# Kernel tuning notes

Hardware: AMD Instinct MI355X
Metric: run time of the kernel (lower is better)

The kernel has to match this reference:

```python
import jax, jax.numpy as jnp
import numpy as np

THRESHOLD = 8.0
BN_EPS = 1e-5


def setup_inputs() -> dict:
    key = jax.random.key(0)
    k1, k2 = jax.random.split(key)
    B, C, H, W = 2, 128, 64, 64
    x = jax.random.normal(k1, (B, C, H, W), dtype=jnp.float32)
    W_fc = jax.random.normal(k2, (C, C), dtype=jnp.float32) * (1.0 / np.sqrt(C))
    b_fc = jnp.zeros((C,), dtype=jnp.float32)
    gamma = jnp.ones((C,), dtype=jnp.float32)
    beta = jnp.zeros((C,), dtype=jnp.float32)
    return {"x": x, "W_fc": W_fc, "b_fc": b_fc, "gamma": gamma, "beta": beta}


def _mean_agg(X, path):
    # X: [B,N,C], path: [B,N,N] (col->row). out = rownorm(path) @ X
    out = jnp.matmul(path, X)
    s = jnp.sum(path, axis=2, keepdims=True)  # [B,N,1]
    norm = jnp.where(s > 0, 1.0 / s, 0.0)     # inf -> 0 as in torch code
    return norm * out


def reference(x, W_fc, b_fc, gamma, beta):
    b, c, h, w = x.shape
    N = h * w
    # [B,N,C] token features
    xf = jnp.transpose(x.reshape(b, c, N), (0, 2, 1))
    # pairwise euclidean distance (cdist, p=2)
    sq = jnp.sum(xf * xf, axis=-1)  # [B,N]
    d2 = sq[:, :, None] + sq[:, None, :] - 2.0 * jnp.einsum('bnc,bmc->bnm', xf, xf)
    dist = jnp.sqrt(jnp.maximum(d2, 0.0))
    Hg = (dist < THRESHOLD).astype(xf.dtype)  # [B,N,N] hypergraph incidence
    # HyperGraphConv: y = fc(x); E = mean(H^T @ y); out = mean(H @ E); res = y + out
    y = jnp.einsum('bnc,dc->bnd', xf, W_fc) + b_fc
    E = _mean_agg(y, jnp.swapaxes(Hg, 1, 2))
    x_out = _mean_agg(E, Hg)
    xe = y + x_out  # [B,N,C]
    # back to [B,C,H,W]
    xo = jnp.transpose(xe, (0, 2, 1)).reshape(b, c, h, w)
    # BatchNorm2d (training mode: batch stats over B,H,W) + SiLU
    mean = jnp.mean(xo, axis=(0, 2, 3), keepdims=True)
    var = jnp.var(xo, axis=(0, 2, 3), keepdims=True)
    xn = (xo - mean) * jax.lax.rsqrt(var + BN_EPS)
    xn = gamma[None, :, None, None] * xn + beta[None, :, None, None]
    return xn * jax.nn.sigmoid(xn)
```

## Files before the change

### kernel.cpp

```cpp
#include <hip/hip_runtime.h>

typedef unsigned short ushort_t;
typedef unsigned int   uint32;
typedef unsigned long long u64;
typedef __bf16 bf16_t;
typedef bf16_t bf16x8 __attribute__((ext_vector_type(8)));
typedef float  f32x4  __attribute__((ext_vector_type(4)));

#define N_TOK 4096
#define C_DIM 128
#define NTOT  8192
#define THRESH2 64.0f

#define XF_OFF  (0u)
#define YF_OFF  (2u<<20)
#define EF_OFF  (6u<<20)
#define XE_OFF  (10u<<20)
#define SQ_OFF  (14u<<20)
#define BN_OFF  ((14u<<20) + 32768u)
#define HB_OFF  (16u<<20)
#define WS_NEED ((size_t)(24u<<20))

__device__ __forceinline__ float b2f(ushort_t u){ return __uint_as_float(((uint32)u)<<16); }
__device__ __forceinline__ ushort_t f2b(float f){
    uint32 u = __float_as_uint(f);
    u += 0x7fffu + ((u>>16)&1u);
    return (ushort_t)(u>>16);
}
__device__ __forceinline__ u64 shfl_u64(u64 v, int src){
    uint32 lo = (uint32)v, hi = (uint32)(v>>32);
    lo = __shfl(lo, src); hi = __shfl(hi, src);
    return ((u64)hi<<32)|lo;
}
__device__ __forceinline__ u64 shfl_xor_u64(u64 v, int m){
    uint32 lo = (uint32)v, hi = (uint32)(v>>32);
    lo = __shfl_xor(lo, m); hi = __shfl_xor(hi, m);
    return ((u64)hi<<32)|lo;
}

__global__ __launch_bounds__(256) void k_fc(const float* __restrict__ x,
                                            const float* __restrict__ W,
                                            const float* __restrict__ bfc,
                                            ushort_t* __restrict__ Xf,
                                            float* __restrict__ Yf,
                                            float* __restrict__ sq,
                                            float* __restrict__ bnp){
    __shared__ ushort_t Xs[64*136];
    __shared__ ushort_t Ws[64*136];
    int tid = threadIdx.x;
    int t0 = blockIdx.x * 64;
    int dh = blockIdx.y;
    int b  = t0 >> 12;
    int n0 = t0 & 4095;
    if (blockIdx.x == 0 && dh == 0){
        #pragma unroll
        for (int k=0;k<8;k++) bnp[tid + 256*k] = 0.f;
    }
    const float* xb = x + (size_t)b * C_DIM * N_TOK + n0;
    #pragma unroll
    for (int k=0;k<8;k++){
        int idx = tid + 256*k;
        int c = idx >> 4, n4 = (idx & 15)*4;
        float4 v = *(const float4*)(xb + (size_t)c*N_TOK + n4);
        Xs[(n4+0)*136 + c] = f2b(v.x);
        Xs[(n4+1)*136 + c] = f2b(v.y);
        Xs[(n4+2)*136 + c] = f2b(v.z);
        Xs[(n4+3)*136 + c] = f2b(v.w);
    }
    const float* Wb = W + (size_t)dh*64*C_DIM;
    #pragma unroll
    for (int k=0;k<8;k++){
        int idx = tid + 256*k;
        int d = idx >> 5, c4 = (idx & 31)*4;
        float4 v = *(const float4*)(Wb + d*C_DIM + c4);
        uint2 u;
        u.x = (uint32)f2b(v.x) | ((uint32)f2b(v.y)<<16);
        u.y = (uint32)f2b(v.z) | ((uint32)f2b(v.w)<<16);
        *(uint2*)(&Ws[d*136 + c4]) = u;
    }
    __syncthreads();
    #pragma unroll
    for (int k=0;k<2;k++){
        int idx = tid + 256*(k + 2*dh);
        int row = idx >> 4, c8 = (idx & 15)*8;
        uint4 o = *(const uint4*)(&Xs[row*136 + c8]);
        *(uint4*)(Xf + (size_t)(t0 + row)*C_DIM + c8) = o;
    }
    if (dh == 0){
        int tok = tid >> 2, p = tid & 3;
        const ushort_t* xr = &Xs[tok*136 + p*32];
        float sacc = 0.f;
        #pragma unroll
        for (int i=0;i<16;i++){
            uint32 u = *(const uint32*)(&xr[i*2]);
            float v0 = __uint_as_float(u<<16);
            float v1 = __uint_as_float(u & 0xffff0000u);
            sacc = fmaf(v0, v0, sacc);
            sacc = fmaf(v1, v1, sacc);
        }
        sacc += __shfl_xor(sacc, 1);
        sacc += __shfl_xor(sacc, 2);
        if (p == 0) sq[t0 + tok] = sacc;
    }
    int wv = tid >> 6, lane = tid & 63;
    int qd = lane >> 4, m = lane & 15;
    f32x4 acc[4] = {{0,0,0,0},{0,0,0,0},{0,0,0,0},{0,0,0,0}};
    #pragma unroll
    for (int kc=0;kc<4;kc++){
        bf16x8 af = *(const bf16x8*)(&Xs[(wv*16 + m)*136 + kc*32 + qd*8]);
        #pragma unroll
        for (int ct=0;ct<4;ct++){
            bf16x8 bfr = *(const bf16x8*)(&Ws[(ct*16+m)*136 + kc*32 + qd*8]);
            acc[ct] = __builtin_amdgcn_mfma_f32_16x16x32_bf16(af, bfr, acc[ct], 0, 0, 0);
        }
    }
    int row = t0 + wv*16 + qd*4;
    #pragma unroll
    for (int ct=0;ct<4;ct++){
        int d = dh*64 + ct*16 + m;
        float bias = bfc[d];
        #pragma unroll
        for (int r=0;r<4;r++)
            Yf[(size_t)(row + r)*C_DIM + d] = acc[ct][r] + bias;
    }
}

__global__ __launch_bounds__(256) void k_gram(const ushort_t* __restrict__ Xf,
                                              const float* __restrict__ sq,
                                              u64* __restrict__ Hb){
    __shared__ ushort_t Al[128*136];
    __shared__ ushort_t Bl[64*136];
    __shared__ u64 rowW[128];
    __shared__ u64 part[256];
    int tid = threadIdx.x;
    int L = blockIdx.x, b = blockIdx.y;
    int bi = (int)((65.0f - sqrtf(4225.0f - 4.0f*(float)L)) * 0.5f);
    while (bi > 0 && bi*(65-bi) > L) --bi;
    while ((bi+1)*(65-(bi+1)) <= L) ++bi;
    int bj = L - bi*(65-bi) + 2*bi;
    int i0 = bi*128, j0 = bj*64;
    const ushort_t* XfA = Xf + (size_t)(b*N_TOK + i0)*C_DIM;
    const ushort_t* XfB = Xf + (size_t)(b*N_TOK + j0)*C_DIM;
    #pragma unroll
    for (int k=0;k<8;k++){
        int q = tid + 256*k;
        int row = q >> 4, cp = (q & 15)*8;
        *(uint4*)(&Al[row*136 + cp]) = *(const uint4*)(XfA + row*C_DIM + cp);
    }
    #pragma unroll
    for (int k=0;k<4;k++){
        int q = tid + 256*k;
        int row = q >> 4, cp = (q & 15)*8;
        *(uint4*)(&Bl[row*136 + cp]) = *(const uint4*)(XfB + row*C_DIM + cp);
    }
    __syncthreads();
    int wv = tid >> 6, lane = tid & 63;
    int qd = lane >> 4, m = lane & 15;
    f32x4 acc[2][4] = {{{0,0,0,0},{0,0,0,0},{0,0,0,0},{0,0,0,0}},
                       {{0,0,0,0},{0,0,0,0},{0,0,0,0},{0,0,0,0}}};
    #pragma unroll
    for (int kc=0;kc<4;kc++){
        bf16x8 a0 = *(const bf16x8*)(&Al[(wv*32 +      m)*136 + kc*32 + qd*8]);
        bf16x8 a1 = *(const bf16x8*)(&Al[(wv*32 + 16 + m)*136 + kc*32 + qd*8]);
        #pragma unroll
        for (int ct=0;ct<4;ct++){
            bf16x8 bfr = *(const bf16x8*)(&Bl[(ct*16+m)*136 + kc*32 + qd*8]);
            acc[0][ct] = __builtin_amdgcn_mfma_f32_16x16x32_bf16(a0, bfr, acc[0][ct], 0, 0, 0);
            acc[1][ct] = __builtin_amdgcn_mfma_f32_16x16x32_bf16(a1, bfr, acc[1][ct], 0, 0, 0);
        }
    }
    float sqj[4];
    #pragma unroll
    for (int ct=0;ct<4;ct++) sqj[ct] = sq[b*N_TOK + j0 + ct*16 + m];
    #pragma unroll
    for (int rt=0;rt<2;rt++){
        int lr = wv*32 + rt*16 + qd*4;
        int ib = i0 + lr;
        float sqi[4];
        #pragma unroll
        for (int r=0;r<4;r++) sqi[r] = sq[b*N_TOK + ib + r];
        #pragma unroll
        for (int r=0;r<4;r++){
            u64 bits = 0;
            #pragma unroll
            for (int ct=0;ct<4;ct++){
                float d2 = sqi[r] + sqj[ct] - 2.0f*acc[rt][ct][r];
                if (d2 < THRESH2) bits |= (u64)1 << (ct*16 + m);
            }
            bits |= shfl_xor_u64(bits, 1);
            bits |= shfl_xor_u64(bits, 2);
            bits |= shfl_xor_u64(bits, 4);
            bits |= shfl_xor_u64(bits, 8);
            if (m == 0){
                Hb[(size_t)(b*N_TOK + ib + r)*64 + bj] = bits;
                rowW[lr + r] = bits;
            }
        }
    }
    __syncthreads();
    {
        int jj = tid & 63, hw = (tid>>6)&1, sub = tid>>7;
        u64 p = 0;
        int ibase = hw*64 + sub*32;
        #pragma unroll 8
        for (int ii=0; ii<32; ii++){
            u64 wrd = rowW[ibase + ii];
            p |= ((wrd >> jj) & 1ull) << (sub*32 + ii);
        }
        part[tid] = p;
    }
    __syncthreads();
    if (tid < 128){
        int jj = tid & 63, hw = tid >> 6;
        u64 wt = part[tid] | part[tid + 128];
        Hb[(size_t)(b*N_TOK + j0 + jj)*64 + 2*bi + hw] = wt;
    }
}

template<int MODE>
__global__ __launch_bounds__(256) void k_aggs(const u64* __restrict__ Hb,
                                              const float* __restrict__ V,
                                              const float* __restrict__ Yf,
                                              float* __restrict__ Out,
                                              float* __restrict__ bnp){
    __shared__ float r1[4][128];
    __shared__ float r2[4][128];
    int tid = threadIdx.x;
    int wv = tid >> 6, lane = tid & 63;
    int row = blockIdx.x * 4 + wv;
    int b = row >> 12;
    u64 myw = Hb[(size_t)row*64 + lane];
    int cnt = __builtin_popcountll(myw);
    cnt += __shfl_xor(cnt, 1);
    cnt += __shfl_xor(cnt, 2);
    cnt += __shfl_xor(cnt, 4);
    cnt += __shfl_xor(cnt, 8);
    cnt += __shfl_xor(cnt, 16);
    cnt += __shfl_xor(cnt, 32);
    float acc0 = 0.f, acc1 = 0.f;
    const float* Vb = V + (size_t)b*N_TOK*C_DIM;
    u64 nz = __ballot(myw != 0);
    while (nz){
        int wdi = __builtin_ctzll(nz);
        nz &= nz - 1;
        u64 mw = shfl_u64(myw, wdi);
        while (mw){
            int j = wdi*64 + __builtin_ctzll(mw);
            mw &= mw - 1;
            acc0 += Vb[(size_t)j*C_DIM + lane];
            acc1 += Vb[(size_t)j*C_DIM + lane + 64];
        }
    }
    float norm = (cnt > 0) ? (1.0f/(float)cnt) : 0.0f;
    size_t o = (size_t)row*C_DIM;
    if (MODE == 0){
        Out[o + lane]      = acc0*norm;
        Out[o + lane + 64] = acc1*norm;
    } else {
        float xe0 = Yf[o + lane]      + acc0*norm;
        float xe1 = Yf[o + lane + 64] + acc1*norm;
        Out[o + lane]      = xe0;
        Out[o + lane + 64] = xe1;
        r1[wv][lane]      = xe0;
        r1[wv][lane + 64] = xe1;
        r2[wv][lane]      = xe0*xe0;
        r2[wv][lane + 64] = xe1*xe1;
        __syncthreads();
        if (tid < 128){
            float s1 = r1[0][tid]+r1[1][tid]+r1[2][tid]+r1[3][tid];
            float s2 = r2[0][tid]+r2[1][tid]+r2[2][tid]+r2[3][tid];
            int prt = blockIdx.x & 7;
            atomicAdd(&bnp[prt*256 + tid],       s1);
            atomicAdd(&bnp[prt*256 + 128 + tid], s2);
        }
    }
}

__global__ __launch_bounds__(256) void k_out(const float* __restrict__ Xe,
                                             const float* __restrict__ bnp,
                                             const float* __restrict__ gamma,
                                             const float* __restrict__ beta,
                                             float* __restrict__ out){
    __shared__ float tile[32][33];
    int tx = threadIdx.x, ty = threadIdx.y;
    int n0 = blockIdx.x*32, c0 = blockIdx.y*32, b = blockIdx.z;
    int c = c0 + tx;
    float s1 = 0.f, s2 = 0.f;
    #pragma unroll
    for (int p=0;p<8;p++){
        s1 += bnp[p*256 + c];
        s2 += bnp[p*256 + 128 + c];
    }
    float inv = 1.0f / (float)NTOT;
    float mean = s1 * inv;
    float var  = s2*inv - mean*mean;
    float scale = gamma[c] * rsqrtf(var + 1e-5f);
    float shift = beta[c] - mean*scale;
    #pragma unroll
    for (int k=0;k<4;k++){
        int nl = ty + 8*k;
        float v = Xe[(size_t)(b*N_TOK + n0 + nl)*C_DIM + c];
        v = scale*v + shift;
        float sg = 1.0f/(1.0f + __expf(-v));
        tile[tx][nl] = v * sg;
    }
    __syncthreads();
    #pragma unroll
    for (int k=0;k<4;k++){
        int cl = ty + 8*k;
        out[(size_t)(b*C_DIM + c0 + cl)*N_TOK + n0 + tx] = tile[cl][tx];
    }
}

extern "C" void kernel_launch(void* const* d_in, const int* in_sizes, int n_in,
                              void* d_out, int out_size, void* d_ws, size_t ws_size,
                              hipStream_t stream){
    if (ws_size < WS_NEED) return;
    const float* x     = (const float*)d_in[0];
    const float* W     = (const float*)d_in[1];
    const float* bfc   = (const float*)d_in[2];
    const float* gamma = (const float*)d_in[3];
    const float* beta  = (const float*)d_in[4];
    char* ws = (char*)d_ws;
    ushort_t* Xf = (ushort_t*)(ws + XF_OFF);
    float*    Yf = (float*)(ws + YF_OFF);
    float*    Ef = (float*)(ws + EF_OFF);
    float*    Xe = (float*)(ws + XE_OFF);
    float*    sq = (float*)(ws + SQ_OFF);
    float*    bnp= (float*)(ws + BN_OFF);
    u64*      Hb = (u64*)(ws + HB_OFF);
    float* out = (float*)d_out;

    k_fc<<<dim3(128,2), dim3(256), 0, stream>>>(x, W, bfc, Xf, Yf, sq, bnp);
    k_gram<<<dim3(1056,2), dim3(256), 0, stream>>>(Xf, sq, Hb);
    k_aggs<0><<<dim3(2048), dim3(256), 0, stream>>>(Hb, Yf, Yf, Ef, bnp);
    k_aggs<1><<<dim3(2048), dim3(256), 0, stream>>>(Hb, Ef, Yf, Xe, bnp);
    k_out<<<dim3(128,4,2), dim3(32,8), 0, stream>>>(Xe, bnp, gamma, beta, out);
}
```

Measured before the change: 112.7 us.

## Fuse all stages into one persistent cooperative kernel with grid syncs

Replaces the five separate launches (fc, gram/threshold bitmask, two aggregations, batchnorm+SiLU) with a single cooperative kernel of 512 blocks that walks through the stages using grid.sync barriers and grid-stride loops over work items. The aim is to remove per-launch overhead and the idle gaps between kernels. The cost is fewer resident blocks per stage, serialization at each grid barrier, and a union of shared memory sized for the largest stage, which may lower occupancy. The previous multi-launch path stays as a fallback when cooperative launch is unavailable.

```diff
diff --git a/kernel.cpp b/kernel.cpp
--- a/kernel.cpp
+++ b/kernel.cpp
@@ -1,4 +1,7 @@
 #include <hip/hip_runtime.h>
+#include <hip/hip_cooperative_groups.h>
+
+namespace cg = cooperative_groups;
 
 typedef unsigned short ushort_t;
 typedef unsigned int   uint32;
@@ -11,6 +14,7 @@
 #define C_DIM 128
 #define NTOT  8192
 #define THRESH2 64.0f
+#define NBLK 512
 
 #define XF_OFF  (0u)
 #define YF_OFF  (2u<<20)
@@ -36,6 +40,317 @@
     uint32 lo = (uint32)v, hi = (uint32)(v>>32);
     lo = __shfl_xor(lo, m); hi = __shfl_xor(hi, m);
     return ((u64)hi<<32)|lo;
+}
+
+union SMem {
+    struct { ushort_t Xs[64*136]; ushort_t Ws[64*136]; } fc;
+    struct { ushort_t Al[128*136]; ushort_t Bl[64*136]; u64 rowW[128]; u64 part[256]; } gr;
+    struct { float r1[4][128]; float r2[4][128]; } agg;
+    struct { float tile[32][33]; } bn;
+};
+
+__global__ __launch_bounds__(256, 2) void k_fused(const float* __restrict__ x,
+                                                  const float* __restrict__ W,
+                                                  const float* __restrict__ bfc,
+                                                  const float* __restrict__ gamma,
+                                                  const float* __restrict__ beta,
+                                                  ushort_t* __restrict__ Xf,
+                                                  float* __restrict__ Yf,
+                                                  float* __restrict__ Ef,
+                                                  float* __restrict__ Xe,
+                                                  float* __restrict__ sq,
+                                                  float* __restrict__ bnp,
+                                                  u64* __restrict__ Hb,
+                                                  float* __restrict__ out){
+    __shared__ SMem sm;
+    cg::grid_group grid = cg::this_grid();
+    int tid = threadIdx.x;
+    int bid = blockIdx.x;
+
+    if (bid < 256){
+        int t0 = (bid >> 1) * 64;
+        int dh = bid & 1;
+        int b  = t0 >> 12;
+        int n0 = t0 & 4095;
+        if (bid == 0){
+            #pragma unroll
+            for (int k=0;k<8;k++) bnp[tid + 256*k] = 0.f;
+        }
+        const float* xb = x + (size_t)b * C_DIM * N_TOK + n0;
+        #pragma unroll
+        for (int k=0;k<8;k++){
+            int idx = tid + 256*k;
+            int c = idx >> 4, n4 = (idx & 15)*4;
+            float4 v = *(const float4*)(xb + (size_t)c*N_TOK + n4);
+            sm.fc.Xs[(n4+0)*136 + c] = f2b(v.x);
+            sm.fc.Xs[(n4+1)*136 + c] = f2b(v.y);
+            sm.fc.Xs[(n4+2)*136 + c] = f2b(v.z);
+            sm.fc.Xs[(n4+3)*136 + c] = f2b(v.w);
+        }
+        const float* Wb = W + (size_t)dh*64*C_DIM;
+        #pragma unroll
+        for (int k=0;k<8;k++){
+            int idx = tid + 256*k;
+            int d = idx >> 5, c4 = (idx & 31)*4;
+            float4 v = *(const float4*)(Wb + d*C_DIM + c4);
+            uint2 u;
+            u.x = (uint32)f2b(v.x) | ((uint32)f2b(v.y)<<16);
+            u.y = (uint32)f2b(v.z) | ((uint32)f2b(v.w)<<16);
+            *(uint2*)(&sm.fc.Ws[d*136 + c4]) = u;
+        }
+        __syncthreads();
+        #pragma unroll
+        for (int k=0;k<2;k++){
+            int idx = tid + 256*(k + 2*dh);
+            int row = idx >> 4, c8 = (idx & 15)*8;
+            uint4 o = *(const uint4*)(&sm.fc.Xs[row*136 + c8]);
+            *(uint4*)(Xf + (size_t)(t0 + row)*C_DIM + c8) = o;
+        }
+        if (dh == 0){
+            int tok = tid >> 2, p = tid & 3;
+            const ushort_t* xr = &sm.fc.Xs[tok*136 + p*32];
+            float sacc = 0.f;
+            #pragma unroll
+            for (int i=0;i<16;i++){
+                uint32 u = *(const uint32*)(&xr[i*2]);
+                float v0 = __uint_as_float(u<<16);
+                float v1 = __uint_as_float(u & 0xffff0000u);
+                sacc = fmaf(v0, v0, sacc);
+                sacc = fmaf(v1, v1, sacc);
+            }
+            sacc += __shfl_xor(sacc, 1);
+            sacc += __shfl_xor(sacc, 2);
+            if (p == 0) sq[t0 + tok] = sacc;
+        }
+        int wv = tid >> 6, lane = tid & 63;
+        int qd = lane >> 4, m = lane & 15;
+        f32x4 acc[4] = {{0,0,0,0},{0,0,0,0},{0,0,0,0},{0,0,0,0}};
+        #pragma unroll
+        for (int kc=0;kc<4;kc++){
+            bf16x8 af = *(const bf16x8*)(&sm.fc.Xs[(wv*16 + m)*136 + kc*32 + qd*8]);
+            #pragma unroll
+            for (int ct=0;ct<4;ct++){
+                bf16x8 bfr = *(const bf16x8*)(&sm.fc.Ws[(ct*16+m)*136 + kc*32 + qd*8]);
+                acc[ct] = __builtin_amdgcn_mfma_f32_16x16x32_bf16(af, bfr, acc[ct], 0, 0, 0);
+            }
+        }
+        int row = t0 + wv*16 + qd*4;
+        #pragma unroll
+        for (int ct=0;ct<4;ct++){
+            int d = dh*64 + ct*16 + m;
+            float bias = bfc[d];
+            #pragma unroll
+            for (int r=0;r<4;r++)
+                Yf[(size_t)(row + r)*C_DIM + d] = acc[ct][r] + bias;
+        }
+    }
+    grid.sync();
+
+    for (int item = bid; item < 2112; item += NBLK){
+        __syncthreads();
+        int bb = (item >= 1056) ? 1 : 0;
+        int L = item - bb*1056;
+        int bi = (int)((65.0f - sqrtf(4225.0f - 4.0f*(float)L)) * 0.5f);
+        while (bi > 0 && bi*(65-bi) > L) --bi;
+        while ((bi+1)*(65-(bi+1)) <= L) ++bi;
+        int bj = L - bi*(65-bi) + 2*bi;
+        int i0 = bi*128, j0 = bj*64;
+        const ushort_t* XfA = Xf + (size_t)(bb*N_TOK + i0)*C_DIM;
+        const ushort_t* XfB = Xf + (size_t)(bb*N_TOK + j0)*C_DIM;
+        #pragma unroll
+        for (int k=0;k<8;k++){
+            int q = tid + 256*k;
+            int row = q >> 4, cp = (q & 15)*8;
+            *(uint4*)(&sm.gr.Al[row*136 + cp]) = *(const uint4*)(XfA + row*C_DIM + cp);
+        }
+        #pragma unroll
+        for (int k=0;k<4;k++){
+            int q = tid + 256*k;
+            int row = q >> 4, cp = (q & 15)*8;
+            *(uint4*)(&sm.gr.Bl[row*136 + cp]) = *(const uint4*)(XfB + row*C_DIM + cp);
+        }
+        __syncthreads();
+        int wv = tid >> 6, lane = tid & 63;
+        int qd = lane >> 4, m = lane & 15;
+        f32x4 acc[2][4] = {{{0,0,0,0},{0,0,0,0},{0,0,0,0},{0,0,0,0}},
+                           {{0,0,0,0},{0,0,0,0},{0,0,0,0},{0,0,0,0}}};
+        #pragma unroll
+        for (int kc=0;kc<4;kc++){
+            bf16x8 a0 = *(const bf16x8*)(&sm.gr.Al[(wv*32 +      m)*136 + kc*32 + qd*8]);
+            bf16x8 a1 = *(const bf16x8*)(&sm.gr.Al[(wv*32 + 16 + m)*136 + kc*32 + qd*8]);
+            #pragma unroll
+            for (int ct=0;ct<4;ct++){
+                bf16x8 bfr = *(const bf16x8*)(&sm.gr.Bl[(ct*16+m)*136 + kc*32 + qd*8]);
+                acc[0][ct] = __builtin_amdgcn_mfma_f32_16x16x32_bf16(a0, bfr, acc[0][ct], 0, 0, 0);
+                acc[1][ct] = __builtin_amdgcn_mfma_f32_16x16x32_bf16(a1, bfr, acc[1][ct], 0, 0, 0);
+            }
+        }
+        float sqj[4];
+        #pragma unroll
+        for (int ct=0;ct<4;ct++) sqj[ct] = sq[bb*N_TOK + j0 + ct*16 + m];
+        #pragma unroll
+        for (int rt=0;rt<2;rt++){
+            int lr = wv*32 + rt*16 + qd*4;
+            int ib = i0 + lr;
+            float sqi[4];
+            #pragma unroll
+            for (int r=0;r<4;r++) sqi[r] = sq[bb*N_TOK + ib + r];
+            #pragma unroll
+            for (int r=0;r<4;r++){
+                u64 bits = 0;
+                #pragma unroll
+                for (int ct=0;ct<4;ct++){
+                    float d2 = sqi[r] + sqj[ct] - 2.0f*acc[rt][ct][r];
+                    if (d2 < THRESH2) bits |= (u64)1 << (ct*16 + m);
+                }
+                bits |= shfl_xor_u64(bits, 1);
+                bits |= shfl_xor_u64(bits, 2);
+                bits |= shfl_xor_u64(bits, 4);
+                bits |= shfl_xor_u64(bits, 8);
+                if (m == 0){
+                    Hb[(size_t)(bb*N_TOK + ib + r)*64 + bj] = bits;
+                    sm.gr.rowW[lr + r] = bits;
+                }
+            }
+        }
+        __syncthreads();
+        {
+            int jj = tid & 63, hw = (tid>>6)&1, sub = tid>>7;
+            u64 p = 0;
+            int ibase = hw*64 + sub*32;
+            #pragma unroll 8
+            for (int ii=0; ii<32; ii++){
+                u64 wrd = sm.gr.rowW[ibase + ii];
+                p |= ((wrd >> jj) & 1ull) << (sub*32 + ii);
+            }
+            sm.gr.part[tid] = p;
+        }
+        __syncthreads();
+        if (tid < 128){
+            int jj = tid & 63, hw = tid >> 6;
+            u64 wt = sm.gr.part[tid] | sm.gr.part[tid + 128];
+            Hb[(size_t)(bb*N_TOK + j0 + jj)*64 + 2*bi + hw] = wt;
+        }
+    }
+    grid.sync();
+
+    {
+        int wv = tid >> 6, lane = tid & 63;
+        u64 myw[4];
+        float nrm[4];
+        #pragma unroll
+        for (int k=0;k<4;k++){
+            int row = (bid + k*NBLK)*4 + wv;
+            u64 w = Hb[(size_t)row*64 + lane];
+            myw[k] = w;
+            int cnt = __builtin_popcountll(w);
+            cnt += __shfl_xor(cnt, 1);
+            cnt += __shfl_xor(cnt, 2);
+            cnt += __shfl_xor(cnt, 4);
+            cnt += __shfl_xor(cnt, 8);
+            cnt += __shfl_xor(cnt, 16);
+            cnt += __shfl_xor(cnt, 32);
+            nrm[k] = (cnt > 0) ? 1.0f/(float)cnt : 0.0f;
+        }
+        #pragma unroll
+        for (int k=0;k<4;k++){
+            int row = (bid + k*NBLK)*4 + wv;
+            int b = row >> 12;
+            const float* Vb = Yf + (size_t)b*N_TOK*C_DIM;
+            float acc0 = 0.f, acc1 = 0.f;
+            u64 nz = __ballot(myw[k] != 0);
+            while (nz){
+                int wdi = __builtin_ctzll(nz);
+                nz &= nz - 1;
+                u64 mw = shfl_u64(myw[k], wdi);
+                while (mw){
+                    int j = wdi*64 + __builtin_ctzll(mw);
+                    mw &= mw - 1;
+                    acc0 += Vb[(size_t)j*C_DIM + lane];
+                    acc1 += Vb[(size_t)j*C_DIM + lane + 64];
+                }
+            }
+            size_t o = (size_t)row*C_DIM;
+            Ef[o + lane]      = acc0*nrm[k];
+            Ef[o + lane + 64] = acc1*nrm[k];
+        }
+        grid.sync();
+        float s1a=0.f, s1b=0.f, s2a=0.f, s2b=0.f;
+        #pragma unroll
+        for (int k=0;k<4;k++){
+            int row = (bid + k*NBLK)*4 + wv;
+            int b = row >> 12;
+            const float* Vb = Ef + (size_t)b*N_TOK*C_DIM;
+            float acc0 = 0.f, acc1 = 0.f;
+            u64 nz = __ballot(myw[k] != 0);
+            while (nz){
+                int wdi = __builtin_ctzll(nz);
+                nz &= nz - 1;
+                u64 mw = shfl_u64(myw[k], wdi);
+                while (mw){
+                    int j = wdi*64 + __builtin_ctzll(mw);
+                    mw &= mw - 1;
+                    acc0 += Vb[(size_t)j*C_DIM + lane];
+                    acc1 += Vb[(size_t)j*C_DIM + lane + 64];
+                }
+            }
+            size_t o = (size_t)row*C_DIM;
+            float xe0 = Yf[o + lane]      + acc0*nrm[k];
+            float xe1 = Yf[o + lane + 64] + acc1*nrm[k];
+            Xe[o + lane]      = xe0;
+            Xe[o + lane + 64] = xe1;
+            s1a += xe0; s2a += xe0*xe0;
+            s1b += xe1; s2b += xe1*xe1;
+        }
+        __syncthreads();
+        sm.agg.r1[wv][lane]      = s1a;
+        sm.agg.r1[wv][lane + 64] = s1b;
+        sm.agg.r2[wv][lane]      = s2a;
+        sm.agg.r2[wv][lane + 64] = s2b;
+        __syncthreads();
+        if (tid < 128){
+            float s1 = sm.agg.r1[0][tid]+sm.agg.r1[1][tid]+sm.agg.r1[2][tid]+sm.agg.r1[3][tid];
+            float s2 = sm.agg.r2[0][tid]+sm.agg.r2[1][tid]+sm.agg.r2[2][tid]+sm.agg.r2[3][tid];
+            int prt = bid & 7;
+            atomicAdd(&bnp[prt*256 + tid],       s1);
+            atomicAdd(&bnp[prt*256 + 128 + tid], s2);
+        }
+    }
+    grid.sync();
+
+    for (int it = bid; it < 1024; it += NBLK){
+        __syncthreads();
+        int bx = it & 127, byz = it >> 7;
+        int by = byz & 3, bz = byz >> 2;
+        int tx = tid & 31, ty = tid >> 5;
+        int n0 = bx*32, c0 = by*32, b = bz;
+        int c = c0 + tx;
+        float s1 = 0.f, s2 = 0.f;
+        #pragma unroll
+        for (int p=0;p<8;p++){
+            s1 += bnp[p*256 + c];
+            s2 += bnp[p*256 + 128 + c];
+        }
+        float inv = 1.0f / (float)NTOT;
+        float mean = s1 * inv;
+        float var  = s2*inv - mean*mean;
+        float scale = gamma[c] * rsqrtf(var + 1e-5f);
+        float shift = beta[c] - mean*scale;
+        #pragma unroll
+        for (int k=0;k<4;k++){
+            int nl = ty + 8*k;
+            float v = Xe[(size_t)(b*N_TOK + n0 + nl)*C_DIM + c];
+            v = scale*v + shift;
+            float sg = 1.0f/(1.0f + __expf(-v));
+            sm.bn.tile[tx][nl] = v * sg;
+        }
+        __syncthreads();
+        #pragma unroll
+        for (int k=0;k<4;k++){
+            int cl = ty + 8*k;
+            out[(size_t)(b*C_DIM + c0 + cl)*N_TOK + n0 + tx] = sm.bn.tile[cl][tx];
+        }
+    }
 }
 
 __global__ __launch_bounds__(256) void k_fc(const float* __restrict__ x,
@@ -326,14 +641,36 @@
     float*    Yf = (float*)(ws + YF_OFF);
     float*    Ef = (float*)(ws + EF_OFF);
     float*    Xe = (float*)(ws + XE_OFF);
-    float*    sq = (float*)(ws + SQ_OFF);
+    float*    sqp= (float*)(ws + SQ_OFF);
     float*    bnp= (float*)(ws + BN_OFF);
     u64*      Hb = (u64*)(ws + HB_OFF);
-    float* out = (float*)d_out;
-
-    k_fc<<<dim3(128,2), dim3(256), 0, stream>>>(x, W, bfc, Xf, Yf, sq, bnp);
-    k_gram<<<dim3(1056,2), dim3(256), 0, stream>>>(Xf, sq, Hb);
+    float*    outp = (float*)d_out;
+
+    static int coop_ok = -1;
+    if (coop_ok < 0){
+        int ok = 0, dev = 0, nb = 0;
+        if (hipGetDevice(&dev) == hipSuccess){
+            hipDeviceProp_t prop;
+            if (hipGetDeviceProperties(&prop, dev) == hipSuccess &&
+                hipOccupancyMaxActiveBlocksPerMultiprocessor(&nb, (const void*)k_fused, 256, 0) == hipSuccess){
+                ok = (prop.cooperativeLaunch != 0) && (nb * prop.multiProcessorCount >= NBLK);
+            }
+        }
+        coop_ok = ok;
+    }
+
+    if (coop_ok){
+        void* args[] = {(void*)&x, (void*)&W, (void*)&bfc, (void*)&gamma, (void*)&beta,
+                        (void*)&Xf, (void*)&Yf, (void*)&Ef, (void*)&Xe, (void*)&sqp,
+                        (void*)&bnp, (void*)&Hb, (void*)&outp};
+        hipError_t e = hipLaunchCooperativeKernel((const void*)k_fused, dim3(NBLK), dim3(256),
+                                                  args, 0, stream);
+        if (e == hipSuccess) return;
+    }
+
+    k_fc<<<dim3(128,2), dim3(256), 0, stream>>>(x, W, bfc, Xf, Yf, sqp, bnp);
+    k_gram<<<dim3(1056,2), dim3(256), 0, stream>>>(Xf, sqp, Hb);
     k_aggs<0><<<dim3(2048), dim3(256), 0, stream>>>(Hb, Yf, Yf, Ef, bnp);
     k_aggs<1><<<dim3(2048), dim3(256), 0, stream>>>(Hb, Ef, Yf, Xe, bnp);
-    k_out<<<dim3(128,4,2), dim3(32,8), 0, stream>>>(Xe, bnp, gamma, beta, out);
-}
+    k_out<<<dim3(128,4,2), dim3(32,8), 0, stream>>>(Xe, bnp, gamma, beta, outp);
+}
```

Measured after the change: 113.1 us. Within noise of the previous version (+0.4%).

## Fuse two hypergraph aggregations into one two-hop kernel and retile gram to 64x64

Applied to the files above, without the earlier changes.

Replaces the two separate aggregation passes (edge mean, then node mean via an intermediate E buffer) with one kernel. For each neighbor j of row i it re-reads j's incidence row, computes its degree, and sums Y over j's neighbors, giving a nested two-hop traversal. This drops the E buffer and one launch but greatly increases per-row work and gathers (roughly degree squared instead of twice the degree). The gram kernel also moves from 128x64 upper-triangular tiles to 64x64 symmetric tiles and skips the transposed write on diagonal tiles.

```diff
diff --git a/kernel.cpp b/kernel.cpp
--- a/kernel.cpp
+++ b/kernel.cpp
@@ -14,14 +14,12 @@
 
 #define XF_OFF  (0u)
 #define YF_OFF  (2u<<20)
-#define EF_OFF  (6u<<20)
 #define XE_OFF  (10u<<20)
 #define SQ_OFF  (14u<<20)
 #define BN_OFF  ((14u<<20) + 32768u)
 #define HB_OFF  (16u<<20)
 #define WS_NEED ((size_t)(24u<<20))
 
-__device__ __forceinline__ float b2f(ushort_t u){ return __uint_as_float(((uint32)u)<<16); }
 __device__ __forceinline__ ushort_t f2b(float f){
     uint32 u = __float_as_uint(f);
     u += 0x7fffu + ((u>>16)&1u);
@@ -36,6 +34,16 @@
     uint32 lo = (uint32)v, hi = (uint32)(v>>32);
     lo = __shfl_xor(lo, m); hi = __shfl_xor(hi, m);
     return ((u64)hi<<32)|lo;
+}
+__device__ __forceinline__ int wave_popc_reduce(u64 w){
+    int cnt = __builtin_popcountll(w);
+    cnt += __shfl_xor(cnt, 1);
+    cnt += __shfl_xor(cnt, 2);
+    cnt += __shfl_xor(cnt, 4);
+    cnt += __shfl_xor(cnt, 8);
+    cnt += __shfl_xor(cnt, 16);
+    cnt += __shfl_xor(cnt, 32);
+    return cnt;
 }
 
 __global__ __launch_bounds__(256) void k_fc(const float* __restrict__ x,
@@ -125,103 +133,87 @@
     }
 }
 
-__global__ __launch_bounds__(256) void k_gram(const ushort_t* __restrict__ Xf,
-                                              const float* __restrict__ sq,
-                                              u64* __restrict__ Hb){
-    __shared__ ushort_t Al[128*136];
+__global__ __launch_bounds__(256) void k_gram64(const ushort_t* __restrict__ Xf,
+                                                const float* __restrict__ sq,
+                                                u64* __restrict__ Hb){
+    __shared__ ushort_t Al[64*136];
     __shared__ ushort_t Bl[64*136];
-    __shared__ u64 rowW[128];
+    __shared__ u64 rowW[64];
     __shared__ u64 part[256];
     int tid = threadIdx.x;
-    int L = blockIdx.x, b = blockIdx.y;
-    int bi = (int)((65.0f - sqrtf(4225.0f - 4.0f*(float)L)) * 0.5f);
-    while (bi > 0 && bi*(65-bi) > L) --bi;
-    while ((bi+1)*(65-(bi+1)) <= L) ++bi;
-    int bj = L - bi*(65-bi) + 2*bi;
-    int i0 = bi*128, j0 = bj*64;
-    const ushort_t* XfA = Xf + (size_t)(b*N_TOK + i0)*C_DIM;
-    const ushort_t* XfB = Xf + (size_t)(b*N_TOK + j0)*C_DIM;
-    #pragma unroll
-    for (int k=0;k<8;k++){
+    int L = blockIdx.x, bb = blockIdx.y;
+    int bi = (int)((129.0f - sqrtf(16641.0f - 8.0f*(float)L)) * 0.5f);
+    while (bi > 0 && bi*(129-bi)/2 > L) --bi;
+    while ((bi+1)*(129-(bi+1))/2 <= L) ++bi;
+    int bj = bi + (L - bi*(129-bi)/2);
+    int i0 = bi*64, j0 = bj*64;
+    const ushort_t* XfA = Xf + (size_t)(bb*N_TOK + i0)*C_DIM;
+    const ushort_t* XfB = Xf + (size_t)(bb*N_TOK + j0)*C_DIM;
+    #pragma unroll
+    for (int k=0;k<4;k++){
         int q = tid + 256*k;
         int row = q >> 4, cp = (q & 15)*8;
         *(uint4*)(&Al[row*136 + cp]) = *(const uint4*)(XfA + row*C_DIM + cp);
-    }
-    #pragma unroll
-    for (int k=0;k<4;k++){
-        int q = tid + 256*k;
-        int row = q >> 4, cp = (q & 15)*8;
         *(uint4*)(&Bl[row*136 + cp]) = *(const uint4*)(XfB + row*C_DIM + cp);
     }
     __syncthreads();
     int wv = tid >> 6, lane = tid & 63;
     int qd = lane >> 4, m = lane & 15;
-    f32x4 acc[2][4] = {{{0,0,0,0},{0,0,0,0},{0,0,0,0},{0,0,0,0}},
-                       {{0,0,0,0},{0,0,0,0},{0,0,0,0},{0,0,0,0}}};
+    f32x4 acc[4] = {{0,0,0,0},{0,0,0,0},{0,0,0,0},{0,0,0,0}};
     #pragma unroll
     for (int kc=0;kc<4;kc++){
-        bf16x8 a0 = *(const bf16x8*)(&Al[(wv*32 +      m)*136 + kc*32 + qd*8]);
-        bf16x8 a1 = *(const bf16x8*)(&Al[(wv*32 + 16 + m)*136 + kc*32 + qd*8]);
+        bf16x8 a0 = *(const bf16x8*)(&Al[(wv*16 + m)*136 + kc*32 + qd*8]);
         #pragma unroll
         for (int ct=0;ct<4;ct++){
             bf16x8 bfr = *(const bf16x8*)(&Bl[(ct*16+m)*136 + kc*32 + qd*8]);
-            acc[0][ct] = __builtin_amdgcn_mfma_f32_16x16x32_bf16(a0, bfr, acc[0][ct], 0, 0, 0);
-            acc[1][ct] = __builtin_amdgcn_mfma_f32_16x16x32_bf16(a1, bfr, acc[1][ct], 0, 0, 0);
+            acc[ct] = __builtin_amdgcn_mfma_f32_16x16x32_bf16(a0, bfr, acc[ct], 0, 0, 0);
         }
     }
     float sqj[4];
     #pragma unroll
-    for (int ct=0;ct<4;ct++) sqj[ct] = sq[b*N_TOK + j0 + ct*16 + m];
-    #pragma unroll
-    for (int rt=0;rt<2;rt++){
-        int lr = wv*32 + rt*16 + qd*4;
-        int ib = i0 + lr;
-        float sqi[4];
-        #pragma unroll
-        for (int r=0;r<4;r++) sqi[r] = sq[b*N_TOK + ib + r];
-        #pragma unroll
-        for (int r=0;r<4;r++){
-            u64 bits = 0;
-            #pragma unroll
-            for (int ct=0;ct<4;ct++){
-                float d2 = sqi[r] + sqj[ct] - 2.0f*acc[rt][ct][r];
-                if (d2 < THRESH2) bits |= (u64)1 << (ct*16 + m);
-            }
-            bits |= shfl_xor_u64(bits, 1);
-            bits |= shfl_xor_u64(bits, 2);
-            bits |= shfl_xor_u64(bits, 4);
-            bits |= shfl_xor_u64(bits, 8);
-            if (m == 0){
-                Hb[(size_t)(b*N_TOK + ib + r)*64 + bj] = bits;
-                rowW[lr + r] = bits;
-            }
-        }
-    }
-    __syncthreads();
-    {
-        int jj = tid & 63, hw = (tid>>6)&1, sub = tid>>7;
+    for (int ct=0;ct<4;ct++) sqj[ct] = sq[bb*N_TOK + j0 + ct*16 + m];
+    int lr = wv*16 + qd*4;
+    int ib = i0 + lr;
+    float sqi[4];
+    #pragma unroll
+    for (int r=0;r<4;r++) sqi[r] = sq[bb*N_TOK + ib + r];
+    #pragma unroll
+    for (int r=0;r<4;r++){
+        u64 bits = 0;
+        #pragma unroll
+        for (int ct=0;ct<4;ct++){
+            float d2 = sqi[r] + sqj[ct] - 2.0f*acc[ct][r];
+            if (d2 < THRESH2) bits |= (u64)1 << (ct*16 + m);
+        }
+        bits |= shfl_xor_u64(bits, 1);
+        bits |= shfl_xor_u64(bits, 2);
+        bits |= shfl_xor_u64(bits, 4);
+        bits |= shfl_xor_u64(bits, 8);
+        if (m == 0){
+            Hb[(size_t)(bb*N_TOK + ib + r)*64 + bj] = bits;
+            rowW[lr + r] = bits;
+        }
+    }
+    __syncthreads();
+    if (bi != bj){
+        int jj = tid & 63, q = tid >> 6;
         u64 p = 0;
-        int ibase = hw*64 + sub*32;
-        #pragma unroll 8
-        for (int ii=0; ii<32; ii++){
-            u64 wrd = rowW[ibase + ii];
-            p |= ((wrd >> jj) & 1ull) << (sub*32 + ii);
-        }
+        int ibase = q*16;
+        #pragma unroll
+        for (int ii=0; ii<16; ii++)
+            p |= ((rowW[ibase + ii] >> jj) & 1ull) << (ibase + ii);
         part[tid] = p;
-    }
-    __syncthreads();
-    if (tid < 128){
-        int jj = tid & 63, hw = tid >> 6;
-        u64 wt = part[tid] | part[tid + 128];
-        Hb[(size_t)(b*N_TOK + j0 + jj)*64 + 2*bi + hw] = wt;
-    }
-}
-
-template<int MODE>
-__global__ __launch_bounds__(256) void k_aggs(const u64* __restrict__ Hb,
-                                              const float* __restrict__ V,
+        __syncthreads();
+        if (tid < 64){
+            u64 wt = part[tid] | part[tid+64] | part[tid+128] | part[tid+192];
+            Hb[(size_t)(bb*N_TOK + j0 + tid)*64 + bi] = wt;
+        }
+    }
+}
+
+__global__ __launch_bounds__(256) void k_agg2(const u64* __restrict__ Hb,
                                               const float* __restrict__ Yf,
-                                              float* __restrict__ Out,
+                                              float* __restrict__ Xe,
                                               float* __restrict__ bnp){
     __shared__ float r1[4][128];
     __shared__ float r2[4][128];
@@ -229,16 +221,11 @@
     int wv = tid >> 6, lane = tid & 63;
     int row = blockIdx.x * 4 + wv;
     int b = row >> 12;
+    const float* Vb = Yf + (size_t)b*N_TOK*C_DIM;
     u64 myw = Hb[(size_t)row*64 + lane];
-    int cnt = __builtin_popcountll(myw);
-    cnt += __shfl_xor(cnt, 1);
-    cnt += __shfl_xor(cnt, 2);
-    cnt += __shfl_xor(cnt, 4);
-    cnt += __shfl_xor(cnt, 8);
-    cnt += __shfl_xor(cnt, 16);
-    cnt += __shfl_xor(cnt, 32);
+    int cnt = wave_popc_reduce(myw);
+    float nrm_i = (cnt > 0) ? 1.0f/(float)cnt : 0.0f;
     float acc0 = 0.f, acc1 = 0.f;
-    const float* Vb = V + (size_t)b*N_TOK*C_DIM;
     u64 nz = __ballot(myw != 0);
     while (nz){
         int wdi = __builtin_ctzll(nz);
@@ -247,32 +234,48 @@
         while (mw){
             int j = wdi*64 + __builtin_ctzll(mw);
             mw &= mw - 1;
-            acc0 += Vb[(size_t)j*C_DIM + lane];
-            acc1 += Vb[(size_t)j*C_DIM + lane + 64];
-        }
-    }
-    float norm = (cnt > 0) ? (1.0f/(float)cnt) : 0.0f;
+            int jrow = (b << 12) + j;
+            u64 jw; float nrm_j;
+            if (jrow == row){
+                jw = myw; nrm_j = nrm_i;
+            } else {
+                jw = Hb[(size_t)jrow*64 + lane];
+                int jc = wave_popc_reduce(jw);
+                nrm_j = (jc > 0) ? 1.0f/(float)jc : 0.0f;
+            }
+            float sub0 = 0.f, sub1 = 0.f;
+            u64 jnz = __ballot(jw != 0);
+            while (jnz){
+                int w2 = __builtin_ctzll(jnz);
+                jnz &= jnz - 1;
+                u64 m2 = shfl_u64(jw, w2);
+                while (m2){
+                    int kk = w2*64 + __builtin_ctzll(m2);
+                    m2 &= m2 - 1;
+                    sub0 += Vb[(size_t)kk*C_DIM + lane];
+                    sub1 += Vb[(size_t)kk*C_DIM + lane + 64];
+                }
+            }
+            acc0 += nrm_j * sub0;
+            acc1 += nrm_j * sub1;
+        }
+    }
     size_t o = (size_t)row*C_DIM;
-    if (MODE == 0){
-        Out[o + lane]      = acc0*norm;
-        Out[o + lane + 64] = acc1*norm;
-    } else {
-        float xe0 = Yf[o + lane]      + acc0*norm;
-        float xe1 = Yf[o + lane + 64] + acc1*norm;
-        Out[o + lane]      = xe0;
-        Out[o + lane + 64] = xe1;
-        r1[wv][lane]      = xe0;
-        r1[wv][lane + 64] = xe1;
-        r2[wv][lane]      = xe0*xe0;
-        r2[wv][lane + 64] = xe1*xe1;
-        __syncthreads();
-        if (tid < 128){
-            float s1 = r1[0][tid]+r1[1][tid]+r1[2][tid]+r1[3][tid];
-            float s2 = r2[0][tid]+r2[1][tid]+r2[2][tid]+r2[3][tid];
-            int prt = blockIdx.x & 7;
-            atomicAdd(&bnp[prt*256 + tid],       s1);
-            atomicAdd(&bnp[prt*256 + 128 + tid], s2);
-        }
+    float xe0 = Yf[o + lane]      + nrm_i*acc0;
+    float xe1 = Yf[o + lane + 64] + nrm_i*acc1;
+    Xe[o + lane]      = xe0;
+    Xe[o + lane + 64] = xe1;
+    r1[wv][lane]      = xe0;
+    r1[wv][lane + 64] = xe1;
+    r2[wv][lane]      = xe0*xe0;
+    r2[wv][lane + 64] = xe1*xe1;
+    __syncthreads();
+    if (tid < 128){
+        float s1 = r1[0][tid]+r1[1][tid]+r1[2][tid]+r1[3][tid];
+        float s2 = r2[0][tid]+r2[1][tid]+r2[2][tid]+r2[3][tid];
+        int prt = blockIdx.x & 7;
+        atomicAdd(&bnp[prt*256 + tid],       s1);
+        atomicAdd(&bnp[prt*256 + 128 + tid], s2);
     }
 }
 
@@ -324,16 +327,14 @@
     char* ws = (char*)d_ws;
     ushort_t* Xf = (ushort_t*)(ws + XF_OFF);
     float*    Yf = (float*)(ws + YF_OFF);
-    float*    Ef = (float*)(ws + EF_OFF);
     float*    Xe = (float*)(ws + XE_OFF);
-    float*    sq = (float*)(ws + SQ_OFF);
+    float*    sqp= (float*)(ws + SQ_OFF);
     float*    bnp= (float*)(ws + BN_OFF);
     u64*      Hb = (u64*)(ws + HB_OFF);
-    float* out = (float*)d_out;
-
-    k_fc<<<dim3(128,2), dim3(256), 0, stream>>>(x, W, bfc, Xf, Yf, sq, bnp);
-    k_gram<<<dim3(1056,2), dim3(256), 0, stream>>>(Xf, sq, Hb);
-    k_aggs<0><<<dim3(2048), dim3(256), 0, stream>>>(Hb, Yf, Yf, Ef, bnp);
-    k_aggs<1><<<dim3(2048), dim3(256), 0, stream>>>(Hb, Ef, Yf, Xe, bnp);
-    k_out<<<dim3(128,4,2), dim3(32,8), 0, stream>>>(Xe, bnp, gamma, beta, out);
-}
+    float*    outp = (float*)d_out;
+
+    k_fc    <<<dim3(128,2),  dim3(256),   0, stream>>>(x, W, bfc, Xf, Yf, sqp, bnp);
+    k_gram64<<<dim3(2080,2), dim3(256),   0, stream>>>(Xf, sqp, Hb);
+    k_agg2  <<<dim3(2048),   dim3(256),   0, stream>>>(Hb, Yf, Xe, bnp);
+    k_out   <<<dim3(128,4,2),dim3(32,8),  0, stream>>>(Xe, bnp, gamma, beta, outp);
+}
```

New measurement: 103.3 us. -8.4%, faster.

## Fuse both hypergraph aggregations into one nested-traversal kernel and swizzle gram LDS

Applied to the files above, without the earlier changes.

The two mean-aggregation passes are merged into a single kernel. For each row it walks its neighbors j, reloads j's incidence bitmask, recomputes j's degree and sums Y over j's neighbors inline. This removes one launch and the intermediate E buffer write and read, but work grows with the square of the degree, which is cheap only when the incidence matrix is very sparse. Separately, the gram kernel's LDS tiles drop row padding in favor of an XOR swizzle to avoid bank conflicts.

```diff
diff --git a/kernel.cpp b/kernel.cpp
--- a/kernel.cpp
+++ b/kernel.cpp
@@ -14,14 +14,12 @@
 
 #define XF_OFF  (0u)
 #define YF_OFF  (2u<<20)
-#define EF_OFF  (6u<<20)
 #define XE_OFF  (10u<<20)
 #define SQ_OFF  (14u<<20)
 #define BN_OFF  ((14u<<20) + 32768u)
 #define HB_OFF  (16u<<20)
 #define WS_NEED ((size_t)(24u<<20))
 
-__device__ __forceinline__ float b2f(ushort_t u){ return __uint_as_float(((uint32)u)<<16); }
 __device__ __forceinline__ ushort_t f2b(float f){
     uint32 u = __float_as_uint(f);
     u += 0x7fffu + ((u>>16)&1u);
@@ -36,6 +34,16 @@
     uint32 lo = (uint32)v, hi = (uint32)(v>>32);
     lo = __shfl_xor(lo, m); hi = __shfl_xor(hi, m);
     return ((u64)hi<<32)|lo;
+}
+__device__ __forceinline__ int wave_popc_reduce(u64 w){
+    int cnt = __builtin_popcountll(w);
+    cnt += __shfl_xor(cnt, 1);
+    cnt += __shfl_xor(cnt, 2);
+    cnt += __shfl_xor(cnt, 4);
+    cnt += __shfl_xor(cnt, 8);
+    cnt += __shfl_xor(cnt, 16);
+    cnt += __shfl_xor(cnt, 32);
+    return cnt;
 }
 
 __global__ __launch_bounds__(256) void k_fc(const float* __restrict__ x,
@@ -128,8 +136,8 @@
 __global__ __launch_bounds__(256) void k_gram(const ushort_t* __restrict__ Xf,
                                               const float* __restrict__ sq,
                                               u64* __restrict__ Hb){
-    __shared__ ushort_t Al[128*136];
-    __shared__ ushort_t Bl[64*136];
+    __shared__ ushort_t Al[128*128];
+    __shared__ ushort_t Bl[64*128];
     __shared__ u64 rowW[128];
     __shared__ u64 part[256];
     int tid = threadIdx.x;
@@ -144,14 +152,16 @@
     #pragma unroll
     for (int k=0;k<8;k++){
         int q = tid + 256*k;
-        int row = q >> 4, cp = (q & 15)*8;
-        *(uint4*)(&Al[row*136 + cp]) = *(const uint4*)(XfA + row*C_DIM + cp);
+        int row = q >> 4, c16 = q & 15;
+        int off = row*256 + ((c16*16) ^ ((row & 7) << 4));
+        *(uint4*)((char*)Al + off) = *(const uint4*)(XfA + row*C_DIM + c16*8);
     }
     #pragma unroll
     for (int k=0;k<4;k++){
         int q = tid + 256*k;
-        int row = q >> 4, cp = (q & 15)*8;
-        *(uint4*)(&Bl[row*136 + cp]) = *(const uint4*)(XfB + row*C_DIM + cp);
+        int row = q >> 4, c16 = q & 15;
+        int off = row*256 + ((c16*16) ^ ((row & 7) << 4));
+        *(uint4*)((char*)Bl + off) = *(const uint4*)(XfB + row*C_DIM + c16*8);
     }
     __syncthreads();
     int wv = tid >> 6, lane = tid & 63;
@@ -160,11 +170,12 @@
                        {{0,0,0,0},{0,0,0,0},{0,0,0,0},{0,0,0,0}}};
     #pragma unroll
     for (int kc=0;kc<4;kc++){
-        bf16x8 a0 = *(const bf16x8*)(&Al[(wv*32 +      m)*136 + kc*32 + qd*8]);
-        bf16x8 a1 = *(const bf16x8*)(&Al[(wv*32 + 16 + m)*136 + kc*32 + qd*8]);
+        int coff = (kc*64 + qd*16) ^ ((m & 7) << 4);
+        bf16x8 a0 = *(const bf16x8*)((char*)Al + (wv*32 +      m)*256 + coff);
+        bf16x8 a1 = *(const bf16x8*)((char*)Al + (wv*32 + 16 + m)*256 + coff);
         #pragma unroll
         for (int ct=0;ct<4;ct++){
-            bf16x8 bfr = *(const bf16x8*)(&Bl[(ct*16+m)*136 + kc*32 + qd*8]);
+            bf16x8 bfr = *(const bf16x8*)((char*)Bl + (ct*16 + m)*256 + coff);
             acc[0][ct] = __builtin_amdgcn_mfma_f32_16x16x32_bf16(a0, bfr, acc[0][ct], 0, 0, 0);
             acc[1][ct] = __builtin_amdgcn_mfma_f32_16x16x32_bf16(a1, bfr, acc[1][ct], 0, 0, 0);
         }
@@ -217,11 +228,9 @@
     }
 }
 
-template<int MODE>
-__global__ __launch_bounds__(256) void k_aggs(const u64* __restrict__ Hb,
-                                              const float* __restrict__ V,
+__global__ __launch_bounds__(256) void k_agg2(const u64* __restrict__ Hb,
                                               const float* __restrict__ Yf,
-                                              float* __restrict__ Out,
+                                              float* __restrict__ Xe,
                                               float* __restrict__ bnp){
     __shared__ float r1[4][128];
     __shared__ float r2[4][128];
@@ -229,16 +238,11 @@
     int wv = tid >> 6, lane = tid & 63;
     int row = blockIdx.x * 4 + wv;
     int b = row >> 12;
+    const float* Vb = Yf + (size_t)b*N_TOK*C_DIM;
     u64 myw = Hb[(size_t)row*64 + lane];
-    int cnt = __builtin_popcountll(myw);
-    cnt += __shfl_xor(cnt, 1);
-    cnt += __shfl_xor(cnt, 2);
-    cnt += __shfl_xor(cnt, 4);
-    cnt += __shfl_xor(cnt, 8);
-    cnt += __shfl_xor(cnt, 16);
-    cnt += __shfl_xor(cnt, 32);
+    int cnt = wave_popc_reduce(myw);
+    float nrm_i = (cnt > 0) ? 1.0f/(float)cnt : 0.0f;
     float acc0 = 0.f, acc1 = 0.f;
-    const float* Vb = V + (size_t)b*N_TOK*C_DIM;
     u64 nz = __ballot(myw != 0);
     while (nz){
         int wdi = __builtin_ctzll(nz);
@@ -247,32 +251,48 @@
         while (mw){
             int j = wdi*64 + __builtin_ctzll(mw);
             mw &= mw - 1;
-            acc0 += Vb[(size_t)j*C_DIM + lane];
-            acc1 += Vb[(size_t)j*C_DIM + lane + 64];
-        }
-    }
-    float norm = (cnt > 0) ? (1.0f/(float)cnt) : 0.0f;
+            int jrow = (b << 12) + j;
+            u64 jw; float nrm_j;
+            if (jrow == row){
+                jw = myw; nrm_j = nrm_i;
+            } else {
+                jw = Hb[(size_t)jrow*64 + lane];
+                int jc = wave_popc_reduce(jw);
+                nrm_j = (jc > 0) ? 1.0f/(float)jc : 0.0f;
+            }
+            float sub0 = 0.f, sub1 = 0.f;
+            u64 jnz = __ballot(jw != 0);
+            while (jnz){
+                int w2 = __builtin_ctzll(jnz);
+                jnz &= jnz - 1;
+                u64 m2 = shfl_u64(jw, w2);
+                while (m2){
+                    int kk = w2*64 + __builtin_ctzll(m2);
+                    m2 &= m2 - 1;
+                    sub0 += Vb[(size_t)kk*C_DIM + lane];
+                    sub1 += Vb[(size_t)kk*C_DIM + lane + 64];
+                }
+            }
+            acc0 += nrm_j * sub0;
+            acc1 += nrm_j * sub1;
+        }
+    }
     size_t o = (size_t)row*C_DIM;
-    if (MODE == 0){
-        Out[o + lane]      = acc0*norm;
-        Out[o + lane + 64] = acc1*norm;
-    } else {
-        float xe0 = Yf[o + lane]      + acc0*norm;
-        float xe1 = Yf[o + lane + 64] + acc1*norm;
-        Out[o + lane]      = xe0;
-        Out[o + lane + 64] = xe1;
-        r1[wv][lane]      = xe0;
-        r1[wv][lane + 64] = xe1;
-        r2[wv][lane]      = xe0*xe0;
-        r2[wv][lane + 64] = xe1*xe1;
-        __syncthreads();
-        if (tid < 128){
-            float s1 = r1[0][tid]+r1[1][tid]+r1[2][tid]+r1[3][tid];
-            float s2 = r2[0][tid]+r2[1][tid]+r2[2][tid]+r2[3][tid];
-            int prt = blockIdx.x & 7;
-            atomicAdd(&bnp[prt*256 + tid],       s1);
-            atomicAdd(&bnp[prt*256 + 128 + tid], s2);
-        }
+    float xe0 = Yf[o + lane]      + nrm_i*acc0;
+    float xe1 = Yf[o + lane + 64] + nrm_i*acc1;
+    Xe[o + lane]      = xe0;
+    Xe[o + lane + 64] = xe1;
+    r1[wv][lane]      = xe0;
+    r1[wv][lane + 64] = xe1;
+    r2[wv][lane]      = xe0*xe0;
+    r2[wv][lane + 64] = xe1*xe1;
+    __syncthreads();
+    if (tid < 128){
+        float s1 = r1[0][tid]+r1[1][tid]+r1[2][tid]+r1[3][tid];
+        float s2 = r2[0][tid]+r2[1][tid]+r2[2][tid]+r2[3][tid];
+        int prt = blockIdx.x & 7;
+        atomicAdd(&bnp[prt*256 + tid],       s1);
+        atomicAdd(&bnp[prt*256 + 128 + tid], s2);
     }
 }
 
@@ -324,16 +344,14 @@
     char* ws = (char*)d_ws;
     ushort_t* Xf = (ushort_t*)(ws + XF_OFF);
     float*    Yf = (float*)(ws + YF_OFF);
-    float*    Ef = (float*)(ws + EF_OFF);
     float*    Xe = (float*)(ws + XE_OFF);
-    float*    sq = (float*)(ws + SQ_OFF);
+    float*    sqp= (float*)(ws + SQ_OFF);
     float*    bnp= (float*)(ws + BN_OFF);
     u64*      Hb = (u64*)(ws + HB_OFF);
-    float* out = (float*)d_out;
-
-    k_fc<<<dim3(128,2), dim3(256), 0, stream>>>(x, W, bfc, Xf, Yf, sq, bnp);
-    k_gram<<<dim3(1056,2), dim3(256), 0, stream>>>(Xf, sq, Hb);
-    k_aggs<0><<<dim3(2048), dim3(256), 0, stream>>>(Hb, Yf, Yf, Ef, bnp);
-    k_aggs<1><<<dim3(2048), dim3(256), 0, stream>>>(Hb, Ef, Yf, Xe, bnp);
-    k_out<<<dim3(128,4,2), dim3(32,8), 0, stream>>>(Xe, bnp, gamma, beta, out);
-}
+    float*    outp = (float*)d_out;
+
+    k_fc  <<<dim3(128,2),  dim3(256),  0, stream>>>(x, W, bfc, Xf, Yf, sqp, bnp);
+    k_gram<<<dim3(1056,2), dim3(256),  0, stream>>>(Xf, sqp, Hb);
+    k_agg2<<<dim3(2048),   dim3(256),  0, stream>>>(Hb, Yf, Xe, bnp);
+    k_out <<<dim3(128,4,2),dim3(32,8), 0, stream>>>(Xe, bnp, gamma, beta, outp);
+}
```

After: 102.6 us. 1.1x faster.
